# Kernel tuning notes

Hardware: AMD Instinct MI355X
Metric: run time of the kernel (lower is better)

The kernel has to match this reference:

```python
import jax, jax.numpy as jnp
import numpy as np

N = 65536   # total nodes
B = 128     # graphs
G = 512     # nodes per graph
E = 65536   # directed edges (before BU flip + self loops)
IN = 512    # in_feats
HID = 64    # hid_feats
OUT = 64    # out_feats
H = 4       # heads (self.K)
NC = 4      # num_class


def _gat(x, src, dst, W, a_src, a_dst, bias, heads, out_ch, concat):
    # PyG GATConv: lin (no bias) -> per-edge LeakyReLU(0.2) attention logits ->
    # softmax over edges grouped by destination -> weighted sum -> +bias.
    n = x.shape[0]
    h = (x @ W).reshape(n, heads, out_ch)            # [N,H,C]
    asrc = (h * a_src).sum(-1)                       # [N,H]
    adst = (h * a_dst).sum(-1)                       # [N,H]
    e = jax.nn.leaky_relu(asrc[src] + adst[dst], 0.2)  # [Etot,H]
    m = jax.ops.segment_max(e, dst, num_segments=n)
    m = jnp.where(jnp.isfinite(m), m, 0.0)
    ex = jnp.exp(e - m[dst])
    den = jax.ops.segment_sum(ex, dst, num_segments=n)
    alpha = ex / den[dst]                            # self-loops guarantee den>0
    out = jax.ops.segment_sum(alpha[:, :, None] * h[src], dst, num_segments=n)
    out = out.reshape(n, heads * out_ch) if concat else out.mean(1)
    return out + bias


def _smean(v, seg, nseg):
    s = jax.ops.segment_sum(v, seg, num_segments=nseg)
    c = jax.ops.segment_sum(jnp.ones((v.shape[0], 1), v.dtype), seg, num_segments=nseg)
    return s / jnp.maximum(c, 1.0)


def setup_inputs() -> dict:
    key = jax.random.key(0)
    ks = jax.random.split(key, 24)
    x = jax.random.normal(ks[0], (N, IN), jnp.float32)
    root = jax.random.normal(ks[1], (B, IN), jnp.float32)
    # edges kept within each graph of G contiguous nodes (PyG batching layout)
    gid = jax.random.randint(ks[2], (E,), 0, B)
    src = gid * G + jax.random.randint(ks[3], (E,), 0, G)
    dst = gid * G + jax.random.randint(ks[4], (E,), 0, G)
    edge_index = jnp.stack([src, dst]).astype(jnp.int32)
    batch = jnp.repeat(jnp.arange(B, dtype=jnp.int32), G)
    ptr = jnp.arange(B + 1, dtype=jnp.int32) * G
    s = 0.05
    r = lambda i, shp: jax.random.normal(ks[i], shp, jnp.float32) * s
    return {
        'x': x, 'root': root, 'edge_index': edge_index, 'batch': batch, 'ptr': ptr,
        'W_post1': r(5, (IN, HID)), 'W_claim1': r(6, (IN, HID)),
        'W1': r(7, (2 * HID, H * HID)), 'att_src1': r(8, (H, HID)),
        'att_dst1': r(9, (H, HID)), 'b1': r(10, (H * HID,)),
        'W_post2': r(11, (HID, HID)), 'W_claim2': r(12, (IN, HID)),
        'W2': r(13, (8 * HID, H * OUT)), 'att_src2': r(14, (H, OUT)),
        'att_dst2': r(15, (H, OUT)), 'b2': r(16, (OUT,)),
        'W_fc': r(17, (4 * OUT, OUT)), 'b_fc': r(18, (OUT,)),
        'W_clf': r(19, (2 * OUT, NC)), 'b_clf': r(20, (NC,)),
    }


def reference(x, root, edge_index, batch, ptr,
              W_post1, W_claim1, W1, att_src1, att_dst1, b1,
              W_post2, W_claim2, W2, att_src2, att_dst2, b2,
              W_fc, b_fc, W_clf, b_clf):
    n = x.shape[0]
    nb = root.shape[0]
    # merged edges: TD + BU (flipped), then self loops (add_self_loops=True)
    merged = jnp.concatenate([edge_index, edge_index[::-1]], axis=1)
    loops = jnp.arange(n, dtype=edge_index.dtype)
    ei = jnp.concatenate([merged, jnp.stack([loops, loops])], axis=1)
    src, dst = ei[0], ei[1]
    # root broadcast (replaces per-batch python loop)
    root_extend = root[batch]                         # [N,IN]
    # PostLevelAttention: gated fusion of node feats and root feats
    h_x = x @ W_post1
    h_c = root_extend @ W_claim1
    g = jax.nn.sigmoid(h_x + h_c)
    h1 = jnp.concatenate([g * h_x + (1 - g) * h_c, h_x], -1)   # [N,2*HID]
    x2 = _gat(h1, src, dst, W1, att_src1, att_dst1, b1, H, HID, True)  # [N,4*HID]
    xr = jax.nn.relu(x2)
    # PostLevelAttention2 on each of the K=4 head slices (vectorized over k)
    hs = jnp.einsum('nkh,hd->nkd', xr.reshape(n, H, HID), W_post2)  # [N,4,HID]
    hc2 = (root_extend @ W_claim2)[:, None, :]                      # [N,1,HID]
    g2 = jax.nn.sigmoid(hs + hc2)
    x3 = jnp.concatenate([g2 * hs + (1 - g2) * hc2, hs], -1).reshape(n, 8 * HID)
    x4 = _gat(x3, src, dst, W2, att_src2, att_dst2, b2, H, OUT, False)  # [N,OUT]
    xr2 = jax.nn.relu(x4)
    # root embedding per graph (x[ptr[i]]) broadcast back to nodes
    h_c3 = xr2[ptr[:-1]][batch]                        # [N,OUT]
    h_joint = jnp.concatenate([h_c3, xr2, xr2 * h_c3, jnp.abs(h_c3 - xr2)], 1)
    beta = jax.nn.softmax(jnp.tanh(h_joint @ W_fc + b_fc), axis=-1)
    s_hat = _smean(beta * xr2, batch, nb)
    s = _smean(xr2, batch, nb)
    logits = jnp.concatenate([s_hat, s], 1) @ W_clf + b_clf
    return jax.nn.log_softmax(logits, axis=1)
```

## Files before the change

kernel.cpp:

```cpp
#include <hip/hip_runtime.h>
#include <math.h>

#define NN   65536
#define BB   128
#define GGR  512
#define EE   65536
#define INF_ 512
#define HIDD 64

typedef __attribute__((ext_vector_type(8))) short bf16x8;
typedef __attribute__((ext_vector_type(4))) float f32x4;
typedef unsigned short ushort_t;
typedef unsigned int uint_t;

static __device__ __forceinline__ float sigmoidf_(float x){ return 1.0f/(1.0f+__expf(-x)); }
static __device__ __forceinline__ float lrelu_(float x){ return x>=0.0f ? x : 0.2f*x; }
static __device__ __forceinline__ float tanhf_(float x){
  float e = __expf(2.f*x);
  return 1.f - 2.f/(e + 1.f);
}

static __device__ __forceinline__ ushort_t f2b(float f){
  union { float f; uint_t u; } v; v.f = f;
  uint_t u = v.u;
  uint_t r = (u + 0x7fffu + ((u >> 16) & 1u)) >> 16;
  return (ushort_t)r;
}
static __device__ __forceinline__ float b2f(uint_t u16){
  union { uint_t u; float f; } v; v.u = u16 << 16; return v.f;
}

static __device__ __forceinline__ void gld16(const void* g, void* l){
  __builtin_amdgcn_global_load_lds((const __attribute__((address_space(1))) void*)g,
                                   (__attribute__((address_space(3))) void*)l, 16, 0, 0);
}

__global__ void k_prep(const float* __restrict__ W1, const float* __restrict__ W2,
                       const float* __restrict__ Wp1, const float* __restrict__ Wp2,
                       const float* __restrict__ Wfc,
                       ushort_t* __restrict__ W1t, ushort_t* __restrict__ W2t,
                       ushort_t* __restrict__ Wp1t, ushort_t* __restrict__ Wp2t,
                       ushort_t* __restrict__ Wfct,
                       const float* __restrict__ root, const float* __restrict__ Wc1,
                       const float* __restrict__ Wc2, float* __restrict__ hc1,
                       float* __restrict__ hc2){
  if (blockIdx.x >= 832){
    int b = blockIdx.x - 832;
    int f = threadIdx.x;
    if (f < 64){
      const float* r = root + (size_t)b*INF_;
      float a1 = 0.f, a2 = 0.f;
      for (int k = 0; k < INF_; ++k){
        float rv = r[k];
        a1 = fmaf(rv, Wc1[k*HIDD+f], a1);
        a2 = fmaf(rv, Wc2[k*HIDD+f], a2);
      }
      hc1[b*HIDD+f] = a1; hc2[b*HIDD+f] = a2;
    }
    return;
  }
  int idx = blockIdx.x*256 + threadIdx.x;
  if (idx < 32768){
    int k = idx >> 8, c = idx & 255;
    W1t[(size_t)c*128 + k] = f2b(W1[idx]);
  } else if (idx < 163840){
    int j = idx - 32768; int k = j >> 8, c = j & 255;
    W2t[(size_t)c*512 + k] = f2b(W2[j]);
  } else if (idx < 196608){
    int j = idx - 163840; int k = j >> 6, c = j & 63;
    Wp1t[(size_t)c*512 + k] = f2b(Wp1[j]);
  } else if (idx < 200704){
    int j = idx - 196608; int k = j >> 6, c = j & 63;
    Wp2t[(size_t)c*64 + k] = f2b(Wp2[j]);
  } else if (idx < 212992){
    int j = idx - 200704; int k = j >> 6, c = j & 63;
    Wfct[(size_t)c*192 + k] = f2b(Wfc[4096 + j]);
  }
}

__global__ __launch_bounds__(256) void k_gemm1_mfma(
    const float* __restrict__ x,
    const ushort_t* __restrict__ Wt,
    const float* __restrict__ hc1,
    ushort_t* __restrict__ h1b){
  constexpr int BK = 128;
  constexpr int ROWB = BK*4;
  __shared__ __align__(16) float As[64*BK];
  int tid = threadIdx.x;
  int w = tid >> 6, lane = tid & 63;
  int lr = lane & 15, lk = lane >> 4;
  int n0 = blockIdx.x * 64;
  int sw = (lr & 7) << 4;
  f32x4 acc[4];
  #pragma unroll
  for (int ci = 0; ci < 4; ++ci) acc[ci] = (f32x4){0.f,0.f,0.f,0.f};
  const char* xg = (const char*)(x + (size_t)n0*512);
  char* Ls = (char*)As;
  const ushort_t* Bb = Wt + (size_t)lr*512 + lk*8;
  int rl = w*16 + lr;
  for (int s = 0; s < 4; ++s){
    #pragma unroll
    for (int i = 0; i < 8; ++i){
      int p = i*4096 + tid*16;
      int row = p >> 9;
      int l = p ^ ((row & 7) << 4);
      gld16(xg + (size_t)row*2048 + s*512 + (l & 511), Ls + p);
    }
    __syncthreads();
    #pragma unroll
    for (int k0 = 0; k0 < BK; k0 += 32){
      int lg = rl*ROWB + (k0 + lk*8)*4;
      float4 fa = *(const float4*)(Ls + (lg ^ sw));
      float4 fb = *(const float4*)(Ls + ((lg + 16) ^ sw));
      bf16x8 af;
      af[0]=(short)f2b(fa.x); af[1]=(short)f2b(fa.y); af[2]=(short)f2b(fa.z); af[3]=(short)f2b(fa.w);
      af[4]=(short)f2b(fb.x); af[5]=(short)f2b(fb.y); af[6]=(short)f2b(fb.z); af[7]=(short)f2b(fb.w);
      #pragma unroll
      for (int ci = 0; ci < 4; ++ci){
        bf16x8 bfv = *(const bf16x8*)(Bb + (size_t)ci*16*512 + s*BK + k0);
        acc[ci] = __builtin_amdgcn_mfma_f32_16x16x32_bf16(af, bfv, acc[ci], 0, 0, 0);
      }
    }
    if (s < 3) __syncthreads();
  }
  int g = n0 >> 9;
  #pragma unroll
  for (int ci = 0; ci < 4; ++ci){
    int col = ci*16 + lr;
    float hc = hc1[g*64 + col];
    #pragma unroll
    for (int q = 0; q < 4; ++q){
      int row = n0 + w*16 + lk*4 + q;
      float hx = acc[ci][q];
      float gg = sigmoidf_(hx + hc);
      float fo = gg*hx + (1.f-gg)*hc;
      h1b[(size_t)row*128 + col]      = f2b(fo);
      h1b[(size_t)row*128 + 64 + col] = f2b(hx);
    }
  }
}

template<int K>
__global__ __launch_bounds__(256) void k_gat_mfma(
    const ushort_t* __restrict__ A,
    const ushort_t* __restrict__ Wt,
    const float* __restrict__ att_s,
    const float* __restrict__ att_d,
    ushort_t* __restrict__ Hout,
    float* __restrict__ asrc,
    float* __restrict__ adst){
  constexpr int BK = (K > 256) ? 256 : K;
  constexpr int NS = K / BK;
  constexpr int ROWB = BK * 2;
  constexpr int RSH = (ROWB == 256) ? 8 : 9;
  __shared__ __align__(16) ushort_t As[64*BK];
  int tid = threadIdx.x;
  int w = tid >> 6, lane = tid & 63;
  int lr = lane & 15, lk = lane >> 4;
  int n0 = blockIdx.x * 64;
  int c0 = w * 64;
  int sw = (lr & 7) << 4;
  f32x4 acc[4][4];
  #pragma unroll
  for (int ri = 0; ri < 4; ++ri)
    #pragma unroll
    for (int ci = 0; ci < 4; ++ci) acc[ri][ci] = (f32x4){0.f,0.f,0.f,0.f};
  const char* Ag = (const char*)(A + (size_t)n0*K);
  char* Ls = (char*)As;
  const ushort_t* Bb = Wt + (size_t)(c0 + lr)*K + lk*8;
  for (int s = 0; s < NS; ++s){
    #pragma unroll
    for (int i = 0; i < (64*ROWB)/4096; ++i){
      int p = i*4096 + tid*16;
      int row = p >> RSH;
      int l = p ^ ((row & 7) << 4);
      gld16(Ag + (size_t)row*(K*2) + s*ROWB + (l & (ROWB-1)), Ls + p);
    }
    __syncthreads();
    #pragma unroll
    for (int k0 = 0; k0 < BK; k0 += 32){
      bf16x8 af[4], bfv[4];
      #pragma unroll
      for (int ri = 0; ri < 4; ++ri){
        int lg = (ri*16 + lr)*ROWB + (k0 + lk*8)*2;
        af[ri] = *(const bf16x8*)(Ls + (lg ^ sw));
      }
      #pragma unroll
      for (int ci = 0; ci < 4; ++ci)
        bfv[ci] = *(const bf16x8*)(Bb + (size_t)ci*16*K + s*BK + k0);
      #pragma unroll
      for (int ri = 0; ri < 4; ++ri)
        #pragma unroll
        for (int ci = 0; ci < 4; ++ci)
          acc[ri][ci] = __builtin_amdgcn_mfma_f32_16x16x32_bf16(af[ri], bfv[ci], acc[ri][ci], 0, 0, 0);
    }
    if (s + 1 < NS) __syncthreads();
  }
  float as_[4], ad_[4];
  #pragma unroll
  for (int ci = 0; ci < 4; ++ci){
    as_[ci] = att_s[c0 + ci*16 + lr];
    ad_[ci] = att_d[c0 + ci*16 + lr];
  }
  #pragma unroll
  for (int ri = 0; ri < 4; ++ri){
    #pragma unroll
    for (int q = 0; q < 4; ++q){
      int row = n0 + ri*16 + lk*4 + q;
      float ps = 0.f, pd = 0.f;
      #pragma unroll
      for (int ci = 0; ci < 4; ++ci){
        float v = acc[ri][ci][q];
        Hout[(size_t)row*256 + c0 + ci*16 + lr] = f2b(v);
        ps = fmaf(v, as_[ci], ps);
        pd = fmaf(v, ad_[ci], pd);
      }
      #pragma unroll
      for (int m = 1; m < 16; m <<= 1){
        ps += __shfl_xor(ps, m);
        pd += __shfl_xor(pd, m);
      }
      if (lr == 0){
        asrc[(size_t)row*4 + w] = ps;
        adst[(size_t)row*4 + w] = pd;
      }
    }
  }
}

__global__ void k_count(const int* __restrict__ ei, int* __restrict__ deg){
  int t = blockIdx.x*256 + threadIdx.x;
  int s = ei[t], d = ei[EE + t];
  atomicAdd(&deg[d], 1);
  atomicAdd(&deg[s], 1);
}

__global__ void k_scan1(const int* __restrict__ deg, int* __restrict__ offa,
                        int* __restrict__ bsum){
  __shared__ int sm[256];
  int tid = threadIdx.x, idx = blockIdx.x*256 + tid;
  int v = deg[idx] + 1;
  sm[tid] = v; __syncthreads();
  for (int o = 1; o < 256; o <<= 1){
    int t = (tid >= o) ? sm[tid-o] : 0;
    __syncthreads();
    sm[tid] += t;
    __syncthreads();
  }
  offa[idx] = sm[tid] - v;
  if (tid == 255) bsum[blockIdx.x] = sm[255];
}

__global__ void k_scan2(int* __restrict__ bsum){
  __shared__ int sm[256];
  int tid = threadIdx.x;
  int v = bsum[tid];
  sm[tid] = v; __syncthreads();
  for (int o = 1; o < 256; o <<= 1){
    int t = (tid >= o) ? sm[tid-o] : 0;
    __syncthreads();
    sm[tid] += t;
    __syncthreads();
  }
  bsum[tid] = sm[tid] - v;
}

__global__ void k_scan3(int* __restrict__ offa, const int* __restrict__ bsum){
  int idx = blockIdx.x*256 + threadIdx.x;
  offa[idx] += bsum[idx >> 8];
}

__global__ void k_fill(const int* __restrict__ ei, const int* __restrict__ offa,
                       int* __restrict__ cur, int* __restrict__ elist){
  int t = blockIdx.x*256 + threadIdx.x;
  int s = ei[t], d = ei[EE + t];
  int p = atomicAdd(&cur[d], 1); elist[offa[d] + p] = s;
  p = atomicAdd(&cur[s], 1);     elist[offa[s] + p] = d;
  p = atomicAdd(&cur[t], 1);     elist[offa[t] + p] = t;
}

template<int LAYER>
__global__ __launch_bounds__(256) void k_agg(const int* __restrict__ offa,
                                             const int* __restrict__ deg,
                                             const int* __restrict__ elist,
                                             const ushort_t* __restrict__ h,
                                             const float* __restrict__ asrc,
                                             const float* __restrict__ adst,
                                             const float* __restrict__ bias,
                                             ushort_t* __restrict__ outb,
                                             float* __restrict__ outf){
  __shared__ float eS[4][4][17][4];
  __shared__ int   sS[4][4][17];
  int bid = blockIdx.x;
  int swz = (bid & 7) * (4096/8) + (bid >> 3);
  int tid = threadIdx.x;
  int wave = tid >> 6, lane = tid & 63;
  int grp = lane >> 4, l = lane & 15;
  int n = swz*16 + wave*4 + grp;
  int o0 = offa[n], cnt = deg[n] + 1;
  float4 adv = *(const float4*)&adst[(size_t)n*4];
  float ad[4] = {adv.x, adv.y, adv.z, adv.w};
  int lim = (cnt < 16) ? cnt : 16;
  int s_l = elist[o0 + ((l < cnt) ? l : 0)];
  float4 asv = *(const float4*)&asrc[(size_t)s_l*4];
  float e_l[4];
  e_l[0] = lrelu_(asv.x + ad[0]); e_l[1] = lrelu_(asv.y + ad[1]);
  e_l[2] = lrelu_(asv.z + ad[2]); e_l[3] = lrelu_(asv.w + ad[3]);
  if (l < lim){
    sS[wave][grp][l] = s_l;
    *(float4*)&eS[wave][grp][l][0] = make_float4(e_l[0], e_l[1], e_l[2], e_l[3]);
  }
  float m[4];
  #pragma unroll
  for (int hh = 0; hh < 4; ++hh) m[hh] = (l < cnt) ? e_l[hh] : -1e30f;
  for (int i = 16 + l; i < cnt; i += 16){
    int s = elist[o0 + i];
    float4 a2 = *(const float4*)&asrc[(size_t)s*4];
    m[0] = fmaxf(m[0], lrelu_(a2.x + ad[0]));
    m[1] = fmaxf(m[1], lrelu_(a2.y + ad[1]));
    m[2] = fmaxf(m[2], lrelu_(a2.z + ad[2]));
    m[3] = fmaxf(m[3], lrelu_(a2.w + ad[3]));
  }
  #pragma unroll
  for (int mask = 1; mask < 16; mask <<= 1)
    #pragma unroll
    for (int hh = 0; hh < 4; ++hh) m[hh] = fmaxf(m[hh], __shfl_xor(m[hh], mask));
  int myh = l >> 2;
  float mm = m[myh];
  float den = 0.f;
  float accv[16] = {};
  for (int i = 0; i < lim; ++i){
    int s = sS[wave][grp][i];
    float e = eS[wave][grp][i][myh];
    float ex = __expf(e - mm);
    den += ex;
    const uint4* hp = (const uint4*)(h + (size_t)s*256 + l*16);
    uint4 h0 = hp[0], h1v = hp[1];
    uint_t uu[8] = {h0.x, h0.y, h0.z, h0.w, h1v.x, h1v.y, h1v.z, h1v.w};
    #pragma unroll
    for (int r = 0; r < 8; ++r){
      accv[2*r+0] = fmaf(ex, b2f(uu[r] & 0xffffu), accv[2*r+0]);
      accv[2*r+1] = fmaf(ex, b2f(uu[r] >> 16),     accv[2*r+1]);
    }
  }
  for (int i = 16; i < cnt; ++i){
    int s = elist[o0 + i];
    float4 a2 = *(const float4*)&asrc[(size_t)s*4];
    float e = lrelu_(((const float*)&a2)[myh] + ad[myh]);
    float ex = __expf(e - mm);
    den += ex;
    const uint4* hp = (const uint4*)(h + (size_t)s*256 + l*16);
    uint4 h0 = hp[0], h1v = hp[1];
    uint_t uu[8] = {h0.x, h0.y, h0.z, h0.w, h1v.x, h1v.y, h1v.z, h1v.w};
    #pragma unroll
    for (int r = 0; r < 8; ++r){
      accv[2*r+0] = fmaf(ex, b2f(uu[r] & 0xffffu), accv[2*r+0]);
      accv[2*r+1] = fmaf(ex, b2f(uu[r] >> 16),     accv[2*r+1]);
    }
  }
  float inv = 1.0f / den;
  if (LAYER == 1){
    #pragma unroll
    for (int r = 0; r < 4; ++r){
      int c = l*16 + r*4;
      float4 bv = *(const float4*)&bias[c];
      float o0v = fmaxf(accv[r*4+0]*inv + bv.x, 0.f);
      float o1v = fmaxf(accv[r*4+1]*inv + bv.y, 0.f);
      float o2v = fmaxf(accv[r*4+2]*inv + bv.z, 0.f);
      float o3v = fmaxf(accv[r*4+3]*inv + bv.w, 0.f);
      uint2 pk;
      pk.x = (uint_t)f2b(o0v) | ((uint_t)f2b(o1v) << 16);
      pk.y = (uint_t)f2b(o2v) | ((uint_t)f2b(o3v) << 16);
      *(uint2*)&outb[(size_t)n*256 + c] = pk;
    }
  } else {
    #pragma unroll
    for (int r = 0; r < 16; ++r) accv[r] *= inv;
    #pragma unroll
    for (int r = 0; r < 16; ++r){
      accv[r] += __shfl_xor(accv[r], 4);
      accv[r] += __shfl_xor(accv[r], 8);
    }
    if (l < 4){
      #pragma unroll
      for (int r = 0; r < 4; ++r){
        int c = l*16 + r*4;
        float4 bv = *(const float4*)&bias[c];
        float4 o;
        o.x = fmaxf(accv[r*4+0]*0.25f + bv.x, 0.f);
        o.y = fmaxf(accv[r*4+1]*0.25f + bv.y, 0.f);
        o.z = fmaxf(accv[r*4+2]*0.25f + bv.z, 0.f);
        o.w = fmaxf(accv[r*4+3]*0.25f + bv.w, 0.f);
        *(float4*)&outf[(size_t)n*64 + c] = o;
      }
    }
  }
}

__global__ __launch_bounds__(256) void k_post2_mfma(
    const ushort_t* __restrict__ xrb,
    const ushort_t* __restrict__ Wp2t,
    const float* __restrict__ hc2,
    ushort_t* __restrict__ x3b){
  int tid = threadIdx.x;
  int w = tid >> 6, lane = tid & 63;
  int lr = lane & 15, lk = lane >> 4;
  int n0 = blockIdx.x * 64;
  int g = n0 >> 9;
  f32x4 acc[4][4];
  #pragma unroll
  for (int ri = 0; ri < 4; ++ri)
    #pragma unroll
    for (int ci = 0; ci < 4; ++ci) acc[ri][ci] = (f32x4){0.f,0.f,0.f,0.f};
  const ushort_t* Ab = xrb + (size_t)(n0 + lr)*256 + w*64 + lk*8;
  const ushort_t* Bb = Wp2t + (size_t)lr*64 + lk*8;
  #pragma unroll
  for (int k0 = 0; k0 < 64; k0 += 32){
    bf16x8 af[4], bfv[4];
    #pragma unroll
    for (int ri = 0; ri < 4; ++ri)
      af[ri] = *(const bf16x8*)(Ab + (size_t)ri*16*256 + k0);
    #pragma unroll
    for (int ci = 0; ci < 4; ++ci)
      bfv[ci] = *(const bf16x8*)(Bb + (size_t)ci*16*64 + k0);
    #pragma unroll
    for (int ri = 0; ri < 4; ++ri)
      #pragma unroll
      for (int ci = 0; ci < 4; ++ci)
        acc[ri][ci] = __builtin_amdgcn_mfma_f32_16x16x32_bf16(af[ri], bfv[ci], acc[ri][ci], 0, 0, 0);
  }
  #pragma unroll
  for (int ci = 0; ci < 4; ++ci){
    int col = ci*16 + lr;
    float hc = hc2[g*64 + col];
    #pragma unroll
    for (int ri = 0; ri < 4; ++ri){
      #pragma unroll
      for (int q = 0; q < 4; ++q){
        int row = n0 + ri*16 + lk*4 + q;
        float a = acc[ri][ci][q];
        float gg = sigmoidf_(a + hc);
        x3b[(size_t)row*512 + w*128 + col]      = f2b(gg*a + (1.f-gg)*hc);
        x3b[(size_t)row*512 + w*128 + 64 + col] = f2b(a);
      }
    }
  }
}

__global__ void k_base(const float* __restrict__ xr2, const float* __restrict__ Wfc,
                       const float* __restrict__ bfc, float* __restrict__ baseS){
  int g = blockIdx.x, c = threadIdx.x;
  const float* r = xr2 + (size_t)g*GGR*64;
  float b = bfc[c];
  for (int j = 0; j < 64; ++j) b = fmaf(r[j], Wfc[j*64 + c], b);
  baseS[g*64 + c] = b;
}

__global__ __launch_bounds__(256) void k_pool_mfma(
    const float* __restrict__ xr2,
    const ushort_t* __restrict__ Wfct,
    const float* __restrict__ baseS,
    float* __restrict__ shat,
    float* __restrict__ ssum){
  __shared__ __align__(16) float xs[64][68];
  __shared__ float rls[64];
  __shared__ float bs[64];
  __shared__ float ls_sh[64];
  __shared__ float ls_s[64];
  int tid = threadIdx.x;
  int n0 = blockIdx.x * 64;
  int g = n0 >> 9;
  {
    int row = tid >> 4, col4 = (tid & 15) * 4;
    #pragma unroll
    for (int i = 0; i < 4; ++i){
      float4 v = *(const float4*)&xr2[(size_t)(n0 + row + i*16)*64 + col4];
      *(float4*)&xs[row + i*16][col4] = v;
    }
    if (tid < 16){
      float4 v = *(const float4*)&xr2[(size_t)((size_t)g*GGR)*64 + tid*4];
      *(float4*)&rls[tid*4] = v;
    }
    if (tid >= 64 && tid < 128) bs[tid-64] = baseS[g*64 + (tid-64)];
    if (tid >= 128 && tid < 192){ ls_sh[tid-128] = 0.f; ls_s[tid-128] = 0.f; }
  }
  __syncthreads();
  int w = tid >> 6, lane = tid & 63;
  int lr = lane & 15, lk = lane >> 4;
  f32x4 acc[4];
  #pragma unroll
  for (int ci = 0; ci < 4; ++ci) acc[ci] = (f32x4){0.f,0.f,0.f,0.f};
  int arow = w*16 + lr;
  #pragma unroll
  for (int k0 = 0; k0 < 192; k0 += 32){
    int seg = k0 >> 6;
    int cb = (k0 & 63) + lk*8;
    bf16x8 af;
    #pragma unroll
    for (int j = 0; j < 8; ++j){
      float xv = xs[arow][cb + j];
      float rv = rls[cb + j];
      float v = (seg == 0) ? xv : (seg == 1 ? xv*rv : fabsf(rv - xv));
      af[j] = (short)f2b(v);
    }
    #pragma unroll
    for (int ci = 0; ci < 4; ++ci){
      bf16x8 bfv = *(const bf16x8*)(Wfct + (size_t)(ci*16+lr)*192 + k0 + lk*8);
      acc[ci] = __builtin_amdgcn_mfma_f32_16x16x32_bf16(af, bfv, acc[ci], 0, 0, 0);
    }
  }
  float bsv[4];
  #pragma unroll
  for (int ci = 0; ci < 4; ++ci) bsv[ci] = bs[ci*16 + lr];
  float c_sh[4] = {0.f,0.f,0.f,0.f}, c_s[4] = {0.f,0.f,0.f,0.f};
  #pragma unroll
  for (int q = 0; q < 4; ++q){
    int rrow = w*16 + lk*4 + q;
    float t[4];
    float mx = -1e30f;
    #pragma unroll
    for (int ci = 0; ci < 4; ++ci){
      t[ci] = tanhf_(acc[ci][q] + bsv[ci]);
      mx = fmaxf(mx, t[ci]);
    }
    #pragma unroll
    for (int mask = 1; mask < 16; mask <<= 1) mx = fmaxf(mx, __shfl_xor(mx, mask));
    float e[4], s = 0.f;
    #pragma unroll
    for (int ci = 0; ci < 4; ++ci){ e[ci] = __expf(t[ci] - mx); s += e[ci]; }
    #pragma unroll
    for (int mask = 1; mask < 16; mask <<= 1) s += __shfl_xor(s, mask);
    float invs = 1.0f / s;
    #pragma unroll
    for (int ci = 0; ci < 4; ++ci){
      float xv = xs[rrow][ci*16 + lr];
      c_sh[ci] = fmaf(e[ci]*invs, xv, c_sh[ci]);
      c_s[ci] += xv;
    }
  }
  #pragma unroll
  for (int ci = 0; ci < 4; ++ci){
    c_sh[ci] += __shfl_xor(c_sh[ci], 16); c_sh[ci] += __shfl_xor(c_sh[ci], 32);
    c_s[ci]  += __shfl_xor(c_s[ci], 16);  c_s[ci]  += __shfl_xor(c_s[ci], 32);
  }
  if (lk == 0){
    #pragma unroll
    for (int ci = 0; ci < 4; ++ci){
      atomicAdd(&ls_sh[ci*16 + lr], c_sh[ci]);
      atomicAdd(&ls_s[ci*16 + lr], c_s[ci]);
    }
  }
  __syncthreads();
  if (tid < 64){
    atomicAdd(&shat[g*64 + tid], ls_sh[tid]);
    atomicAdd(&ssum[g*64 + tid], ls_s[tid]);
  }
}

__global__ void k_final(const float* __restrict__ shat, const float* __restrict__ ssum,
                        const float* __restrict__ Wc, const float* __restrict__ bc,
                        float* __restrict__ outp){
  int g = threadIdx.x;
  float l0 = bc[0], l1 = bc[1], l2 = bc[2], l3 = bc[3];
  const float s512 = 1.0f/512.0f;
  for (int j = 0; j < 64; ++j){
    float sh = shat[g*64 + j]*s512;
    float ss = ssum[g*64 + j]*s512;
    float4 w1 = *(const float4*)&Wc[j*4];
    float4 w2 = *(const float4*)&Wc[(64+j)*4];
    l0 = fmaf(sh, w1.x, fmaf(ss, w2.x, l0));
    l1 = fmaf(sh, w1.y, fmaf(ss, w2.y, l1));
    l2 = fmaf(sh, w1.z, fmaf(ss, w2.z, l2));
    l3 = fmaf(sh, w1.w, fmaf(ss, w2.w, l3));
  }
  float mx = fmaxf(fmaxf(l0,l1), fmaxf(l2,l3));
  float s = __expf(l0-mx)+__expf(l1-mx)+__expf(l2-mx)+__expf(l3-mx);
  float lse = mx + logf(s);
  outp[g*4+0] = l0 - lse;
  outp[g*4+1] = l1 - lse;
  outp[g*4+2] = l2 - lse;
  outp[g*4+3] = l3 - lse;
}

extern "C" void kernel_launch(void* const* d_in, const int* in_sizes, int n_in,
                              void* d_out, int out_size, void* d_ws, size_t ws_size,
                              hipStream_t stream){
  const float* x        = (const float*)d_in[0];
  const float* root     = (const float*)d_in[1];
  const int*   ei       = (const int*)d_in[2];
  const float* W_post1  = (const float*)d_in[5];
  const float* W_claim1 = (const float*)d_in[6];
  const float* W1       = (const float*)d_in[7];
  const float* att_src1 = (const float*)d_in[8];
  const float* att_dst1 = (const float*)d_in[9];
  const float* b1       = (const float*)d_in[10];
  const float* W_post2  = (const float*)d_in[11];
  const float* W_claim2 = (const float*)d_in[12];
  const float* W2       = (const float*)d_in[13];
  const float* att_src2 = (const float*)d_in[14];
  const float* att_dst2 = (const float*)d_in[15];
  const float* b2       = (const float*)d_in[16];
  const float* W_fc     = (const float*)d_in[17];
  const float* b_fc     = (const float*)d_in[18];
  const float* W_clf    = (const float*)d_in[19];
  const float* b_clf    = (const float*)d_in[20];
  float* out = (float*)d_out;

  char* w = (char*)d_ws;
  size_t o = 0;
  auto alloc = [&](size_t bytes)->char*{ char* p = w + o; o += (bytes + 255) & ~(size_t)255; return p; };
  ushort_t* RA   = (ushort_t*)alloc((size_t)NN*512*2);
  ushort_t* RB   = (ushort_t*)alloc((size_t)NN*256*2);
  ushort_t* xrb  = (ushort_t*)alloc((size_t)NN*256*2);
  float* xr2  = (float*)alloc((size_t)NN*64*4);
  float* asrc = (float*)alloc((size_t)NN*4*4);
  float* adst = (float*)alloc((size_t)NN*4*4);
  float* hc1  = (float*)alloc(128*64*4);
  float* hc2  = (float*)alloc(128*64*4);
  float* baseS= (float*)alloc(128*64*4);
  ushort_t* W1t  = (ushort_t*)alloc((size_t)256*128*2);
  ushort_t* W2t  = (ushort_t*)alloc((size_t)256*512*2);
  ushort_t* Wp1t = (ushort_t*)alloc((size_t)64*512*2);
  ushort_t* Wp2t = (ushort_t*)alloc((size_t)64*64*2);
  ushort_t* Wfct = (ushort_t*)alloc((size_t)64*192*2);
  int*   deg  = (int*)alloc((size_t)NN*4);
  int*   cur  = (int*)alloc((size_t)NN*4);
  int*   offa = (int*)alloc((size_t)NN*4);
  int*   bsum = (int*)alloc(256*4);
  int*   elist= (int*)alloc((size_t)(2*EE+NN)*4);
  float* shat = (float*)alloc(128*64*4);
  float* ssumv= (float*)alloc(128*64*4);

  ushort_t* h1b = RA;
  ushort_t* x3b = RA;
  ushort_t* h2b = RB;
  ushort_t* h3b = RB;

  hipMemsetAsync(deg,  0, (size_t)NN*8, stream);
  hipMemsetAsync(shat, 0, 2*128*64*4 + 256, stream);


  k_prep<<<960, 256, 0, stream>>>(W1, W2, W_post1, W_post2, W_fc,
                                  W1t, W2t, Wp1t, Wp2t, Wfct,
                                  root, W_claim1, W_claim2, hc1, hc2);
  k_gemm1_mfma<<<1024, 256, 0, stream>>>(x, Wp1t, hc1, h1b);
  k_gat_mfma<128><<<1024, 256, 0, stream>>>(h1b, W1t, att_src1, att_dst1, h2b, asrc, adst);
  k_count<<<256, 256, 0, stream>>>(ei, deg);
  k_scan1<<<256, 256, 0, stream>>>(deg, offa, bsum);
  k_scan2<<<1, 256, 0, stream>>>(bsum);
  k_scan3<<<256, 256, 0, stream>>>(offa, bsum);
  k_fill<<<256, 256, 0, stream>>>(ei, offa, cur, elist);
  k_agg<1><<<4096, 256, 0, stream>>>(offa, deg, elist, h2b, asrc, adst, b1, xrb, nullptr);
  k_post2_mfma<<<1024, 256, 0, stream>>>(xrb, Wp2t, hc2, x3b);
  k_gat_mfma<512><<<1024, 256, 0, stream>>>(x3b, W2t, att_src2, att_dst2, h3b, asrc, adst);
  k_agg<2><<<4096, 256, 0, stream>>>(offa, deg, elist, h3b, asrc, adst, b2, nullptr, xr2);
  k_base<<<128, 64, 0, stream>>>(xr2, W_fc, b_fc, baseS);
  k_pool_mfma<<<1024, 256, 0, stream>>>(xr2, Wfct, baseS, shat, ssumv);
  k_final<<<1, 128, 0, stream>>>(shat, ssumv, W_clf, b_clf, out);
  (void)in_sizes; (void)n_in; (void)out_size; (void)ws_size;
}
```

Baseline: 278.9 us.

## Fuse gated projection with GAT linear layers and fold base into pooling

Merges the first gated projection GEMM with the layer-1 GAT linear GEMM so the intermediate h1 tile stays in shared memory instead of going through global memory. Likewise fuses the post-level attention projection with the layer-2 GAT GEMM, producing x3 per head in LDS and accumulating directly into the output. It also removes k_base by having each pooling block compute its graph's root bias term itself. This cuts global round-trips of large bf16 intermediates and three launches, at the cost of more LDS per block (possible occupancy loss) and redundant base computation across blocks.

Result: faster. 263.8 us (-5.4%).

```diff
diff --git a/kernel.cpp b/kernel.cpp
--- a/kernel.cpp
+++ b/kernel.cpp
@@ -78,25 +78,28 @@
   }
 }
 
-__global__ __launch_bounds__(256) void k_gemm1_mfma(
+__global__ __launch_bounds__(256) void k_l1(
     const float* __restrict__ x,
-    const ushort_t* __restrict__ Wt,
+    const ushort_t* __restrict__ Wp1t,
     const float* __restrict__ hc1,
-    ushort_t* __restrict__ h1b){
-  constexpr int BK = 128;
-  constexpr int ROWB = BK*4;
-  __shared__ __align__(16) float As[64*BK];
+    const ushort_t* __restrict__ W1t,
+    const float* __restrict__ att_s, const float* __restrict__ att_d,
+    ushort_t* __restrict__ Hout,
+    float* __restrict__ asrc, float* __restrict__ adst){
+  __shared__ __align__(16) float xs[64*128];
+  __shared__ __align__(16) ushort_t h1s[64*128];
   int tid = threadIdx.x;
   int w = tid >> 6, lane = tid & 63;
   int lr = lane & 15, lk = lane >> 4;
   int n0 = blockIdx.x * 64;
+  int g = n0 >> 9;
   int sw = (lr & 7) << 4;
-  f32x4 acc[4];
-  #pragma unroll
-  for (int ci = 0; ci < 4; ++ci) acc[ci] = (f32x4){0.f,0.f,0.f,0.f};
+  f32x4 accA[4];
+  #pragma unroll
+  for (int ci = 0; ci < 4; ++ci) accA[ci] = (f32x4){0.f,0.f,0.f,0.f};
   const char* xg = (const char*)(x + (size_t)n0*512);
-  char* Ls = (char*)As;
-  const ushort_t* Bb = Wt + (size_t)lr*512 + lk*8;
+  char* Ls = (char*)xs;
+  const ushort_t* BbA = Wp1t + (size_t)lr*512 + lk*8;
   int rl = w*16 + lr;
   for (int s = 0; s < 4; ++s){
     #pragma unroll
@@ -108,8 +111,8 @@
     }
     __syncthreads();
     #pragma unroll
-    for (int k0 = 0; k0 < BK; k0 += 32){
-      int lg = rl*ROWB + (k0 + lk*8)*4;
+    for (int k0 = 0; k0 < 128; k0 += 32){
+      int lg = rl*512 + (k0 + lk*8)*4;
       float4 fa = *(const float4*)(Ls + (lg ^ sw));
       float4 fb = *(const float4*)(Ls + ((lg + 16) ^ sw));
       bf16x8 af;
@@ -117,84 +120,166 @@
       af[4]=(short)f2b(fb.x); af[5]=(short)f2b(fb.y); af[6]=(short)f2b(fb.z); af[7]=(short)f2b(fb.w);
       #pragma unroll
       for (int ci = 0; ci < 4; ++ci){
-        bf16x8 bfv = *(const bf16x8*)(Bb + (size_t)ci*16*512 + s*BK + k0);
-        acc[ci] = __builtin_amdgcn_mfma_f32_16x16x32_bf16(af, bfv, acc[ci], 0, 0, 0);
-      }
-    }
-    if (s < 3) __syncthreads();
-  }
-  int g = n0 >> 9;
+        bf16x8 bfv = *(const bf16x8*)(BbA + (size_t)ci*16*512 + s*128 + k0);
+        accA[ci] = __builtin_amdgcn_mfma_f32_16x16x32_bf16(af, bfv, accA[ci], 0, 0, 0);
+      }
+    }
+    __syncthreads();
+  }
+  char* Hc = (char*)h1s;
   #pragma unroll
   for (int ci = 0; ci < 4; ++ci){
     int col = ci*16 + lr;
     float hc = hc1[g*64 + col];
     #pragma unroll
     for (int q = 0; q < 4; ++q){
-      int row = n0 + w*16 + lk*4 + q;
-      float hx = acc[ci][q];
+      int row = w*16 + lk*4 + q;
+      int swr = (row & 7) << 4;
+      float hx = accA[ci][q];
       float gg = sigmoidf_(hx + hc);
       float fo = gg*hx + (1.f-gg)*hc;
-      h1b[(size_t)row*128 + col]      = f2b(fo);
-      h1b[(size_t)row*128 + 64 + col] = f2b(hx);
-    }
-  }
-}
-
-template<int K>
-__global__ __launch_bounds__(256) void k_gat_mfma(
-    const ushort_t* __restrict__ A,
-    const ushort_t* __restrict__ Wt,
-    const float* __restrict__ att_s,
-    const float* __restrict__ att_d,
+      *(ushort_t*)(Hc + ((row*256 + col*2) ^ swr))        = f2b(fo);
+      *(ushort_t*)(Hc + ((row*256 + (64 + col)*2) ^ swr)) = f2b(hx);
+    }
+  }
+  __syncthreads();
+  int c0 = w * 64;
+  f32x4 acc[4][4];
+  #pragma unroll
+  for (int ri = 0; ri < 4; ++ri)
+    #pragma unroll
+    for (int ci = 0; ci < 4; ++ci) acc[ri][ci] = (f32x4){0.f,0.f,0.f,0.f};
+  #pragma unroll
+  for (int k0 = 0; k0 < 128; k0 += 32){
+    bf16x8 af[4], bfv[4];
+    #pragma unroll
+    for (int ri = 0; ri < 4; ++ri){
+      int lg = (ri*16 + lr)*256 + (k0 + lk*8)*2;
+      af[ri] = *(const bf16x8*)(Hc + (lg ^ sw));
+    }
+    #pragma unroll
+    for (int ci = 0; ci < 4; ++ci)
+      bfv[ci] = *(const bf16x8*)(W1t + (size_t)(c0 + ci*16 + lr)*128 + k0 + lk*8);
+    #pragma unroll
+    for (int ri = 0; ri < 4; ++ri)
+      #pragma unroll
+      for (int ci = 0; ci < 4; ++ci)
+        acc[ri][ci] = __builtin_amdgcn_mfma_f32_16x16x32_bf16(af[ri], bfv[ci], acc[ri][ci], 0, 0, 0);
+  }
+  float as_[4], ad_[4];
+  #pragma unroll
+  for (int ci = 0; ci < 4; ++ci){
+    as_[ci] = att_s[c0 + ci*16 + lr];
+    ad_[ci] = att_d[c0 + ci*16 + lr];
+  }
+  #pragma unroll
+  for (int ri = 0; ri < 4; ++ri){
+    #pragma unroll
+    for (int q = 0; q < 4; ++q){
+      int row = n0 + ri*16 + lk*4 + q;
+      float ps = 0.f, pd = 0.f;
+      #pragma unroll
+      for (int ci = 0; ci < 4; ++ci){
+        float v = acc[ri][ci][q];
+        Hout[(size_t)row*256 + c0 + ci*16 + lr] = f2b(v);
+        ps = fmaf(v, as_[ci], ps);
+        pd = fmaf(v, ad_[ci], pd);
+      }
+      #pragma unroll
+      for (int m = 1; m < 16; m <<= 1){
+        ps += __shfl_xor(ps, m);
+        pd += __shfl_xor(pd, m);
+      }
+      if (lr == 0){
+        asrc[(size_t)row*4 + w] = ps;
+        adst[(size_t)row*4 + w] = pd;
+      }
+    }
+  }
+}
+
+__global__ __launch_bounds__(256) void k_l2(
+    const ushort_t* __restrict__ xrb,
+    const ushort_t* __restrict__ Wp2t,
+    const float* __restrict__ hc2,
+    const ushort_t* __restrict__ W2t,
+    const float* __restrict__ att_s, const float* __restrict__ att_d,
     ushort_t* __restrict__ Hout,
-    float* __restrict__ asrc,
-    float* __restrict__ adst){
-  constexpr int BK = (K > 256) ? 256 : K;
-  constexpr int NS = K / BK;
-  constexpr int ROWB = BK * 2;
-  constexpr int RSH = (ROWB == 256) ? 8 : 9;
-  __shared__ __align__(16) ushort_t As[64*BK];
+    float* __restrict__ asrc, float* __restrict__ adst){
+  __shared__ __align__(16) ushort_t xs[64*256];
+  __shared__ __align__(16) ushort_t x3s[64*128];
   int tid = threadIdx.x;
   int w = tid >> 6, lane = tid & 63;
   int lr = lane & 15, lk = lane >> 4;
   int n0 = blockIdx.x * 64;
+  int g = n0 >> 9;
+  int sw = (lr & 7) << 4;
+  char* Xc = (char*)xs;
+  char* Sc = (char*)x3s;
+  {
+    const char* Ag = (const char*)(xrb + (size_t)n0*256);
+    #pragma unroll
+    for (int i = 0; i < 8; ++i){
+      int p = i*4096 + tid*16;
+      int row = p >> 9;
+      int l = p ^ ((row & 7) << 4);
+      gld16(Ag + (size_t)row*512 + (l & 511), Xc + p);
+    }
+  }
+  __syncthreads();
   int c0 = w * 64;
-  int sw = (lr & 7) << 4;
   f32x4 acc[4][4];
   #pragma unroll
   for (int ri = 0; ri < 4; ++ri)
     #pragma unroll
     for (int ci = 0; ci < 4; ++ci) acc[ri][ci] = (f32x4){0.f,0.f,0.f,0.f};
-  const char* Ag = (const char*)(A + (size_t)n0*K);
-  char* Ls = (char*)As;
-  const ushort_t* Bb = Wt + (size_t)(c0 + lr)*K + lk*8;
-  for (int s = 0; s < NS; ++s){
-    #pragma unroll
-    for (int i = 0; i < (64*ROWB)/4096; ++i){
-      int p = i*4096 + tid*16;
-      int row = p >> RSH;
-      int l = p ^ ((row & 7) << 4);
-      gld16(Ag + (size_t)row*(K*2) + s*ROWB + (l & (ROWB-1)), Ls + p);
+  for (int hd = 0; hd < 4; ++hd){
+    f32x4 acc2[4];
+    #pragma unroll
+    for (int ci = 0; ci < 4; ++ci) acc2[ci] = (f32x4){0.f,0.f,0.f,0.f};
+    #pragma unroll
+    for (int k0 = 0; k0 < 64; k0 += 32){
+      int lg = (w*16 + lr)*512 + (hd*64 + k0 + lk*8)*2;
+      bf16x8 af = *(const bf16x8*)(Xc + (lg ^ sw));
+      #pragma unroll
+      for (int ci = 0; ci < 4; ++ci){
+        bf16x8 bfv = *(const bf16x8*)(Wp2t + (size_t)(ci*16 + lr)*64 + k0 + lk*8);
+        acc2[ci] = __builtin_amdgcn_mfma_f32_16x16x32_bf16(af, bfv, acc2[ci], 0, 0, 0);
+      }
+    }
+    #pragma unroll
+    for (int ci = 0; ci < 4; ++ci){
+      int col = ci*16 + lr;
+      float hc = hc2[g*64 + col];
+      #pragma unroll
+      for (int q = 0; q < 4; ++q){
+        int row = w*16 + lk*4 + q;
+        int swr = (row & 7) << 4;
+        float a = acc2[ci][q];
+        float gg = sigmoidf_(a + hc);
+        *(ushort_t*)(Sc + ((row*256 + col*2) ^ swr))        = f2b(gg*a + (1.f-gg)*hc);
+        *(ushort_t*)(Sc + ((row*256 + (64 + col)*2) ^ swr)) = f2b(a);
+      }
     }
     __syncthreads();
     #pragma unroll
-    for (int k0 = 0; k0 < BK; k0 += 32){
+    for (int k0 = 0; k0 < 128; k0 += 32){
       bf16x8 af[4], bfv[4];
       #pragma unroll
       for (int ri = 0; ri < 4; ++ri){
-        int lg = (ri*16 + lr)*ROWB + (k0 + lk*8)*2;
-        af[ri] = *(const bf16x8*)(Ls + (lg ^ sw));
+        int lg = (ri*16 + lr)*256 + (k0 + lk*8)*2;
+        af[ri] = *(const bf16x8*)(Sc + (lg ^ sw));
       }
       #pragma unroll
       for (int ci = 0; ci < 4; ++ci)
-        bfv[ci] = *(const bf16x8*)(Bb + (size_t)ci*16*K + s*BK + k0);
+        bfv[ci] = *(const bf16x8*)(W2t + (size_t)(c0 + ci*16 + lr)*512 + hd*128 + k0 + lk*8);
       #pragma unroll
       for (int ri = 0; ri < 4; ++ri)
         #pragma unroll
         for (int ci = 0; ci < 4; ++ci)
           acc[ri][ci] = __builtin_amdgcn_mfma_f32_16x16x32_bf16(af[ri], bfv[ci], acc[ri][ci], 0, 0, 0);
     }
-    if (s + 1 < NS) __syncthreads();
+    if (hd < 3) __syncthreads();
   }
   float as_[4], ad_[4];
   #pragma unroll
@@ -397,69 +482,11 @@
   }
 }
 
-__global__ __launch_bounds__(256) void k_post2_mfma(
-    const ushort_t* __restrict__ xrb,
-    const ushort_t* __restrict__ Wp2t,
-    const float* __restrict__ hc2,
-    ushort_t* __restrict__ x3b){
-  int tid = threadIdx.x;
-  int w = tid >> 6, lane = tid & 63;
-  int lr = lane & 15, lk = lane >> 4;
-  int n0 = blockIdx.x * 64;
-  int g = n0 >> 9;
-  f32x4 acc[4][4];
-  #pragma unroll
-  for (int ri = 0; ri < 4; ++ri)
-    #pragma unroll
-    for (int ci = 0; ci < 4; ++ci) acc[ri][ci] = (f32x4){0.f,0.f,0.f,0.f};
-  const ushort_t* Ab = xrb + (size_t)(n0 + lr)*256 + w*64 + lk*8;
-  const ushort_t* Bb = Wp2t + (size_t)lr*64 + lk*8;
-  #pragma unroll
-  for (int k0 = 0; k0 < 64; k0 += 32){
-    bf16x8 af[4], bfv[4];
-    #pragma unroll
-    for (int ri = 0; ri < 4; ++ri)
-      af[ri] = *(const bf16x8*)(Ab + (size_t)ri*16*256 + k0);
-    #pragma unroll
-    for (int ci = 0; ci < 4; ++ci)
-      bfv[ci] = *(const bf16x8*)(Bb + (size_t)ci*16*64 + k0);
-    #pragma unroll
-    for (int ri = 0; ri < 4; ++ri)
-      #pragma unroll
-      for (int ci = 0; ci < 4; ++ci)
-        acc[ri][ci] = __builtin_amdgcn_mfma_f32_16x16x32_bf16(af[ri], bfv[ci], acc[ri][ci], 0, 0, 0);
-  }
-  #pragma unroll
-  for (int ci = 0; ci < 4; ++ci){
-    int col = ci*16 + lr;
-    float hc = hc2[g*64 + col];
-    #pragma unroll
-    for (int ri = 0; ri < 4; ++ri){
-      #pragma unroll
-      for (int q = 0; q < 4; ++q){
-        int row = n0 + ri*16 + lk*4 + q;
-        float a = acc[ri][ci][q];
-        float gg = sigmoidf_(a + hc);
-        x3b[(size_t)row*512 + w*128 + col]      = f2b(gg*a + (1.f-gg)*hc);
-        x3b[(size_t)row*512 + w*128 + 64 + col] = f2b(a);
-      }
-    }
-  }
-}
-
-__global__ void k_base(const float* __restrict__ xr2, const float* __restrict__ Wfc,
-                       const float* __restrict__ bfc, float* __restrict__ baseS){
-  int g = blockIdx.x, c = threadIdx.x;
-  const float* r = xr2 + (size_t)g*GGR*64;
-  float b = bfc[c];
-  for (int j = 0; j < 64; ++j) b = fmaf(r[j], Wfc[j*64 + c], b);
-  baseS[g*64 + c] = b;
-}
-
 __global__ __launch_bounds__(256) void k_pool_mfma(
     const float* __restrict__ xr2,
     const ushort_t* __restrict__ Wfct,
-    const float* __restrict__ baseS,
+    const float* __restrict__ Wfc,
+    const float* __restrict__ bfc,
     float* __restrict__ shat,
     float* __restrict__ ssum){
   __shared__ __align__(16) float xs[64][68];
@@ -481,8 +508,13 @@
       float4 v = *(const float4*)&xr2[(size_t)((size_t)g*GGR)*64 + tid*4];
       *(float4*)&rls[tid*4] = v;
     }
-    if (tid >= 64 && tid < 128) bs[tid-64] = baseS[g*64 + (tid-64)];
     if (tid >= 128 && tid < 192){ ls_sh[tid-128] = 0.f; ls_s[tid-128] = 0.f; }
+  }
+  __syncthreads();
+  if (tid < 64){
+    float b = bfc[tid];
+    for (int j = 0; j < 64; ++j) b = fmaf(rls[j], Wfc[j*64 + tid], b);
+    bs[tid] = b;
   }
   __syncthreads();
   int w = tid >> 6, lane = tid & 63;
@@ -609,7 +641,6 @@
   char* w = (char*)d_ws;
   size_t o = 0;
   auto alloc = [&](size_t bytes)->char*{ char* p = w + o; o += (bytes + 255) & ~(size_t)255; return p; };
-  ushort_t* RA   = (ushort_t*)alloc((size_t)NN*512*2);
   ushort_t* RB   = (ushort_t*)alloc((size_t)NN*256*2);
   ushort_t* xrb  = (ushort_t*)alloc((size_t)NN*256*2);
   float* xr2  = (float*)alloc((size_t)NN*64*4);
@@ -617,7 +648,6 @@
   float* adst = (float*)alloc((size_t)NN*4*4);
   float* hc1  = (float*)alloc(128*64*4);
   float* hc2  = (float*)alloc(128*64*4);
-  float* baseS= (float*)alloc(128*64*4);
   ushort_t* W1t  = (ushort_t*)alloc((size_t)256*128*2);
   ushort_t* W2t  = (ushort_t*)alloc((size_t)256*512*2);
   ushort_t* Wp1t = (ushort_t*)alloc((size_t)64*512*2);
@@ -631,31 +661,25 @@
   float* shat = (float*)alloc(128*64*4);
   float* ssumv= (float*)alloc(128*64*4);
 
-  ushort_t* h1b = RA;
-  ushort_t* x3b = RA;
   ushort_t* h2b = RB;
   ushort_t* h3b = RB;
 
   hipMemsetAsync(deg,  0, (size_t)NN*8, stream);
-  hipMemsetAsync(shat, 0, 2*128*64*4 + 256, stream);
-
+  hipMemsetAsync(shat, 0, 2*128*64*4, stream);
 
   k_prep<<<960, 256, 0, stream>>>(W1, W2, W_post1, W_post2, W_fc,
                                   W1t, W2t, Wp1t, Wp2t, Wfct,
                                   root, W_claim1, W_claim2, hc1, hc2);
-  k_gemm1_mfma<<<1024, 256, 0, stream>>>(x, Wp1t, hc1, h1b);
-  k_gat_mfma<128><<<1024, 256, 0, stream>>>(h1b, W1t, att_src1, att_dst1, h2b, asrc, adst);
   k_count<<<256, 256, 0, stream>>>(ei, deg);
   k_scan1<<<256, 256, 0, stream>>>(deg, offa, bsum);
   k_scan2<<<1, 256, 0, stream>>>(bsum);
   k_scan3<<<256, 256, 0, stream>>>(offa, bsum);
   k_fill<<<256, 256, 0, stream>>>(ei, offa, cur, elist);
+  k_l1<<<1024, 256, 0, stream>>>(x, Wp1t, hc1, W1t, att_src1, att_dst1, h2b, asrc, adst);
   k_agg<1><<<4096, 256, 0, stream>>>(offa, deg, elist, h2b, asrc, adst, b1, xrb, nullptr);
-  k_post2_mfma<<<1024, 256, 0, stream>>>(xrb, Wp2t, hc2, x3b);
-  k_gat_mfma<512><<<1024, 256, 0, stream>>>(x3b, W2t, att_src2, att_dst2, h3b, asrc, adst);
+  k_l2<<<1024, 256, 0, stream>>>(xrb, Wp2t, hc2, W2t, att_src2, att_dst2, h3b, asrc, adst);
   k_agg<2><<<4096, 256, 0, stream>>>(offa, deg, elist, h3b, asrc, adst, b2, nullptr, xr2);
-  k_base<<<128, 64, 0, stream>>>(xr2, W_fc, b_fc, baseS);
-  k_pool_mfma<<<1024, 256, 0, stream>>>(xr2, Wfct, baseS, shat, ssumv);
+  k_pool_mfma<<<1024, 256, 0, stream>>>(xr2, Wfct, W_fc, b_fc, shat, ssumv);
   k_final<<<1, 128, 0, stream>>>(shat, ssumv, W_clf, b_clf, out);
   (void)in_sizes; (void)n_in; (void)out_size; (void)ws_size;
 }
```
